# Kernel tuning notes

Hardware: AMD Instinct MI355X
Metric: run time of the kernel (lower is better)

## Reference

```python
import jax, jax.numpy as jnp
import numpy as np

WS = 4        # window_size
SHIFT = 3     # shift_size
HEADS = 4
DIM = 128
HR, WR = 256, 256  # input_resolution (matches post-upsample H, W)


def _rel_pos_index(ws):
    coords = np.stack(np.meshgrid(np.arange(ws), np.arange(ws), indexing='ij'))  # (2, ws, ws)
    cf = coords.reshape(2, -1)
    rel = (cf[:, :, None] - cf[:, None, :]).transpose(1, 2, 0).astype(np.int64)
    rel[:, :, 0] += ws - 1
    rel[:, :, 1] += ws - 1
    rel[:, :, 0] *= 2 * ws - 1
    return rel.sum(-1)  # (N, N)


def _attn_mask(H, W, ws, shift):
    img = np.zeros((H, W))
    cnt = 0
    sl = (slice(0, -ws), slice(-ws, -shift), slice(-shift, None))
    for hs in sl:
        for wsl in sl:
            img[hs, wsl] = cnt
            cnt += 1
    mw = img.reshape(H // ws, ws, W // ws, ws).transpose(0, 2, 1, 3).reshape(-1, ws * ws)
    diff = mw[:, None, :] - mw[:, :, None]  # unsqueeze(1) - unsqueeze(2)
    return np.where(diff != 0, -100.0, 0.0).astype(np.float32)  # (nW, N, N)


REL_IDX = jnp.asarray(_rel_pos_index(WS))
ATTN_MASK = jnp.asarray(_attn_mask(HR, WR, WS, SHIFT))


def _upsample2x_ac(x):
    def interp(x, axis):
        n = x.shape[axis]
        m = 2 * n
        pos = jnp.arange(m) * ((n - 1) / (m - 1))
        lo = jnp.floor(pos).astype(jnp.int32)
        hi = jnp.minimum(lo + 1, n - 1)
        w = (pos - lo).astype(x.dtype)
        shp = [1] * x.ndim
        shp[axis] = m
        w = w.reshape(shp)
        return jnp.take(x, lo, axis=axis) * (1 - w) + jnp.take(x, hi, axis=axis) * w
    return interp(interp(x, 2), 3)


def _conv2d(x, w, b, pad):
    y = jax.lax.conv_general_dilated(x, w, (1, 1), [(pad, pad), (pad, pad)],
                                     dimension_numbers=('NCHW', 'OIHW', 'NCHW'))
    return y + b[None, :, None, None]


def _bn(x, g, b, m, v):
    # eval-mode BatchNorm2d
    s = g / jnp.sqrt(v + 1e-5)
    return x * s[None, :, None, None] + (b - m * s)[None, :, None, None]


def setup_inputs():
    key = jax.random.key(0)
    ks = jax.random.split(key, 8)
    f = jax.random.normal
    return {
        'x': f(ks[0], (4, 256, 128, 64), jnp.float32),
        'qkv_w': f(ks[1], (DIM, 3 * DIM), jnp.float32) * 0.02,
        'qkv_b': jnp.zeros((3 * DIM,), jnp.float32),
        'proj_w': f(ks[2], (DIM, DIM), jnp.float32) * 0.02,
        'proj_b': jnp.zeros((DIM,), jnp.float32),
        'rpb': f(ks[3], ((2 * WS - 1) ** 2, HEADS), jnp.float32) * 0.02,
        'conv1_w': f(ks[4], (256, 256, 3, 3), jnp.float32) * 0.02,
        'conv1_b': jnp.zeros((256,), jnp.float32),
        'bn1_g': jnp.ones((256,), jnp.float32),
        'bn1_b': jnp.zeros((256,), jnp.float32),
        'bn1_m': jnp.zeros((256,), jnp.float32),
        'bn1_v': jnp.ones((256,), jnp.float32),
        'conv2_w': f(ks[5], (256, 256, 3, 3), jnp.float32) * 0.02,
        'conv2_b': jnp.zeros((256,), jnp.float32),
        'bn2_g': jnp.ones((256,), jnp.float32),
        'bn2_b': jnp.zeros((256,), jnp.float32),
        'bn2_m': jnp.zeros((256,), jnp.float32),
        'bn2_v': jnp.ones((256,), jnp.float32),
        'idc_w': f(ks[6], (256, 256, 1, 1), jnp.float32) * 0.02,
        'idc_b': jnp.zeros((256,), jnp.float32),
        'bni_g': jnp.ones((256,), jnp.float32),
        'bni_b': jnp.zeros((256,), jnp.float32),
        'bni_m': jnp.zeros((256,), jnp.float32),
        'bni_v': jnp.ones((256,), jnp.float32),
    }


def reference(x, qkv_w, qkv_b, proj_w, proj_b, rpb,
              conv1_w, conv1_b, bn1_g, bn1_b, bn1_m, bn1_v,
              conv2_w, conv2_b, bn2_g, bn2_b, bn2_m, bn2_v,
              idc_w, idc_b, bni_g, bni_b, bni_m, bni_v):
    x = _upsample2x_ac(x)                 # (B, 256, 256, 128), treated as (B,H,W,C) downstream
    B, H, W, C = x.shape
    shortcut = x
    xs = jnp.roll(x, (-SHIFT, -SHIFT), axis=(1, 2))
    # window partition -> (B*nW, N, C)
    nWh, nWw = H // WS, W // WS
    xw = xs.reshape(B, nWh, WS, nWw, WS, C).transpose(0, 1, 3, 2, 4, 5).reshape(-1, WS * WS, C)
    B_, N, _ = xw.shape
    hd = C // HEADS
    qkv = (xw @ qkv_w + qkv_b).reshape(B_, N, 3, HEADS, hd).transpose(2, 0, 3, 1, 4)
    q, k, v = qkv[0], qkv[1], qkv[2]
    attn = jnp.einsum('bhnd,bhmd->bhnm', q * (hd ** -0.5), k)
    bias = rpb[REL_IDX.reshape(-1)].reshape(N, N, HEADS).transpose(2, 0, 1)  # (h, N, N)
    attn = attn + bias[None]
    nW = ATTN_MASK.shape[0]
    attn = attn.reshape(B_ // nW, nW, HEADS, N, N) + ATTN_MASK[None, :, None]
    attn = jax.nn.softmax(attn.reshape(B_, HEADS, N, N), axis=-1)
    out = jnp.einsum('bhnm,bhmd->bhnd', attn, v).transpose(0, 2, 1, 3).reshape(B_, N, C)
    out = out @ proj_w + proj_b
    # window reverse + roll back
    out = out.reshape(B, nWh, nWw, WS, WS, C).transpose(0, 1, 3, 2, 4, 5).reshape(B, H, W, C)
    out = jnp.roll(out, (SHIFT, SHIFT), axis=(1, 2))
    x = shortcut + out
    # DoubleConv with identity branch (tensor treated as NCHW, per original code)
    y = _conv2d(x, conv1_w, conv1_b, 1)
    y = jax.nn.relu(_bn(y, bn1_g, bn1_b, bn1_m, bn1_v))
    y = _conv2d(y, conv2_w, conv2_b, 1)
    y = _bn(y, bn2_g, bn2_b, bn2_m, bn2_v)
    idn = _bn(_conv2d(x, idc_w, idc_b, 0), bni_g, bni_b, bni_m, bni_v)
    return jax.nn.relu(y + idn)
```

## Files before the change

kernel.cpp:

```cpp
#include <hip/hip_runtime.h>
#include <hip/hip_bf16.h>
#include <math.h>
#include <cstddef>

#define BATCH 4
#define WDIM 256
#define CDIM 128
#define WS 4
#define SHIFT 3
#define HEADS 4
#define HD 32
#define NTOK 16

typedef __attribute__((ext_vector_type(8))) short short8;
typedef __attribute__((ext_vector_type(4))) int int4v;
typedef __attribute__((ext_vector_type(4))) float f32x4;

__device__ __forceinline__ int regionOf(int v) {
    return v < (WDIM - WS) ? 0 : (v < (WDIM - SHIFT) ? 1 : 2);
}

__device__ __forceinline__ short f2bf(float v) {
    __hip_bfloat16 h = __float2bfloat16(v);
    return __builtin_bit_cast(short, h);
}
__device__ __forceinline__ float bf2f(short s) {
    unsigned u = ((unsigned)(unsigned short)s) << 16;
    return __builtin_bit_cast(float, u);
}

__global__ __launch_bounds__(256) void repack_attnw(
    const float* __restrict__ qkv_w,
    const float* __restrict__ proj_w,
    __hip_bfloat16* __restrict__ qkvw_rep,
    __hip_bfloat16* __restrict__ projw_rep)
{
    int idx = blockIdx.x * 256 + threadIdx.x;
    if (idx < 49152) {
        int j = idx >> 7, c = idx & 127;
        qkvw_rep[idx] = __float2bfloat16(qkv_w[c * 384 + j]);
    } else {
        int k = idx - 49152;
        int j = k >> 7, c = k & 127;
        projw_rep[k] = __float2bfloat16(proj_w[c * 128 + j]);
    }
}

#define XROW_RS 2114

__global__ __launch_bounds__(256, 4) void attn_kernel(
    const float* __restrict__ xin,
    const __hip_bfloat16* __restrict__ qkvw_rep,
    const __hip_bfloat16* __restrict__ projw_rep,
    const float* __restrict__ qkv_b,
    const float* __restrict__ proj_b,
    const float* __restrict__ rpb,
    __hip_bfloat16* __restrict__ xatt)
{
    __shared__ __align__(16) char smem[40864];
    float* xrowF  = (float*)smem;
    short* qkvs   = (short*)smem;
    short* aoutS  = (short*)smem;
    short* Xb     = (short*)(smem + 16912);
    short* Ps     = (short*)(smem + 25616);
    short* Vt     = (short*)(smem + 29712);
    float* rpbs   = (float*)(smem + 37904);
    float* qkvbS  = (float*)(smem + 38688);
    float* projbS = (float*)(smem + 40224);
    float* tokw2  = (float*)(smem + 40736);

    const int tid = threadIdx.x;
    const int bid = blockIdx.x;
    const int l   = tid & 63;
    const int wv  = tid >> 6;
    const int lm  = l & 15;
    const int lq  = l >> 4;

    if (tid < 196) rpbs[tid] = rpb[tid];
    for (int i = tid; i < 384; i += 256) qkvbS[i] = qkv_b[i];
    if (tid < 128) projbS[tid] = proj_b[tid];

    #pragma unroll
    for (int k = 0; k < 4; k++) {
        int id = tid + k * 256;
        int n   = id >> 5;
        int row = (id >> 4) & 1;
        int ll  = id & 15;
        int w_  = n >> 4, nn = n & 15;
        int win = bid * 2 + w_;
        int b   = win >> 12;
        int wh  = (win >> 6) & 63;
        int ww  = win & 63;
        int r = nn >> 2, c = nn & 3;
        int gh = (wh * 4 + r + SHIFT) & 255;
        int gw = (ww * 4 + c + SHIFT) & 255;
        float pos2 = gw * (127.0f / 255.0f);
        int lo2 = (int)floorf(pos2);
        int hi2 = min(lo2 + 1, 127);
        if (row == 0 && ll == 0) tokw2[n] = pos2 - (float)lo2;
        int src = row == 0 ? lo2 : hi2;
        const float4* rp = (const float4*)(xin + (((size_t)b * 256 + gh) * 128 + src) * 64);
        float4 v = rp[ll];
        float* bp = xrowF + row * XROW_RS + n + (4 * ll) * 33;
        bp[0]      = v.x;
        bp[33]     = v.y;
        bp[66]     = v.z;
        bp[99]     = v.w;
    }
    __syncthreads();

    {
        int n = tid >> 3;
        int jj = tid & 7;
        float w2 = tokw2[n];
        const float* x0 = xrowF + n;
        const float* x1 = x0 + XROW_RS;
        #pragma unroll
        for (int p = 0; p < 8; p++) {
            unsigned pk = 0;
            #pragma unroll
            for (int q = 0; q < 2; q++) {
                int cc = jj * 16 + p * 2 + q;
                float pos3 = cc * (63.0f / 127.0f);
                int lo3 = (int)floorf(pos3);
                float w3 = pos3 - (float)lo3;
                int o = lo3 * 33;
                float v0 = x0[o] * (1.f - w3) + x0[o + 33] * w3;
                float v1 = x1[o] * (1.f - w3) + x1[o + 33] * w3;
                float out = v0 * (1.f - w2) + v1 * w2;
                pk |= ((unsigned)(unsigned short)f2bf(out)) << (16 * q);
            }
            *(unsigned*)&Xb[n * 136 + jj * 16 + p * 2] = pk;
        }
    }
    __syncthreads();

    {
        f32x4 qacc[6][2];
        #pragma unroll
        for (int a = 0; a < 6; a++)
            #pragma unroll
            for (int t = 0; t < 2; t++) qacc[a][t] = (f32x4)0.0f;

        for (int ks = 0; ks < 4; ks++) {
            short8 af[6];
            #pragma unroll
            for (int jj = 0; jj < 6; jj++) {
                const int4v* gp = (const int4v*)(qkvw_rep +
                    (size_t)(wv * 96 + jj * 16 + lm) * 128 + ks * 32 + lq * 8);
                af[jj] = __builtin_bit_cast(short8, *gp);
            }
            short8 bfr[2];
            #pragma unroll
            for (int tt = 0; tt < 2; tt++)
                bfr[tt] = *(const short8*)&Xb[(tt * 16 + lm) * 136 + ks * 32 + lq * 8];
            #pragma unroll
            for (int jj = 0; jj < 6; jj++)
                #pragma unroll
                for (int tt = 0; tt < 2; tt++)
                    qacc[jj][tt] = __builtin_amdgcn_mfma_f32_16x16x32_bf16(
                        af[jj], bfr[tt], qacc[jj][tt], 0, 0, 0);
        }
        #pragma unroll
        for (int jj = 0; jj < 6; jj++) {
            int jbase = wv * 96 + jj * 16 + lq * 4;
            #pragma unroll
            for (int tt = 0; tt < 2; tt++) {
                int tok = tt * 16 + lm;
                if (jbase < 128) {
                    float v0 = (qacc[jj][tt][0] + qkvbS[jbase+0]) * 0.17677669529663687f;
                    float v1 = (qacc[jj][tt][1] + qkvbS[jbase+1]) * 0.17677669529663687f;
                    float v2 = (qacc[jj][tt][2] + qkvbS[jbase+2]) * 0.17677669529663687f;
                    float v3 = (qacc[jj][tt][3] + qkvbS[jbase+3]) * 0.17677669529663687f;
                    unsigned p0 = (unsigned short)f2bf(v0) | ((unsigned)(unsigned short)f2bf(v1) << 16);
                    unsigned p1 = (unsigned short)f2bf(v2) | ((unsigned)(unsigned short)f2bf(v3) << 16);
                    *(unsigned*)&qkvs[tok * 264 + jbase]     = p0;
                    *(unsigned*)&qkvs[tok * 264 + jbase + 2] = p1;
                } else if (jbase < 256) {
                    float v0 = qacc[jj][tt][0] + qkvbS[jbase+0];
                    float v1 = qacc[jj][tt][1] + qkvbS[jbase+1];
                    float v2 = qacc[jj][tt][2] + qkvbS[jbase+2];
                    float v3 = qacc[jj][tt][3] + qkvbS[jbase+3];
                    unsigned p0 = (unsigned short)f2bf(v0) | ((unsigned)(unsigned short)f2bf(v1) << 16);
                    unsigned p1 = (unsigned short)f2bf(v2) | ((unsigned)(unsigned short)f2bf(v3) << 16);
                    *(unsigned*)&qkvs[tok * 264 + jbase]     = p0;
                    *(unsigned*)&qkvs[tok * 264 + jbase + 2] = p1;
                } else {
                    #pragma unroll
                    for (int r = 0; r < 4; r++) {
                        int d = jbase - 256 + r;
                        Vt[(tt * 128 + d) * 16 + lm] = f2bf(qacc[jj][tt][r] + qkvbS[jbase + r]);
                    }
                }
            }
        }
    }
    __syncthreads();

    {
        int w_ = wv >> 1;
        int hb = (wv & 1) * 2;
        int win = bid * 2 + w_;
        int wh = (win >> 6) & 63;
        int ww = win & 63;
        int nq = lm;
        int r1 = nq >> 2, c1 = nq & 3;
        int reg1 = regionOf(wh * 4 + r1) * 3 + regionOf(ww * 4 + c1);
        #pragma unroll
        for (int hh = 0; hh < 2; hh++) {
            int h = hb + hh;
            short8 qa = *(const short8*)&qkvs[(w_ * 16 + lm) * 264 + h * 32 + lq * 8];
            short8 kb = *(const short8*)&qkvs[(w_ * 16 + lm) * 264 + 128 + h * 32 + lq * 8];
            f32x4 s = __builtin_amdgcn_mfma_f32_16x16x32_bf16(kb, qa, (f32x4)0.0f, 0, 0, 0);
            float v[4];
            #pragma unroll
            for (int r = 0; r < 4; r++) {
                int m = lq * 4 + r;
                int r2 = m >> 2, c2 = m & 3;
                int ridx = (r1 - r2 + 3) * 7 + (c1 - c2 + 3);
                v[r] = s[r] + rpbs[ridx * 4 + h];
                int reg2 = regionOf(wh * 4 + r2) * 3 + regionOf(ww * 4 + c2);
                if (reg2 != reg1) v[r] -= 100.f;
            }
            float mx = fmaxf(fmaxf(v[0], v[1]), fmaxf(v[2], v[3]));
            mx = fmaxf(mx, __shfl_xor(mx, 16));
            mx = fmaxf(mx, __shfl_xor(mx, 32));
            float e0 = __expf(v[0] - mx);
            float e1 = __expf(v[1] - mx);
            float e2 = __expf(v[2] - mx);
            float e3 = __expf(v[3] - mx);
            float ss = (e0 + e1) + (e2 + e3);
            ss += __shfl_xor(ss, 16);
            ss += __shfl_xor(ss, 32);
            float rinv = 1.0f / ss;
            unsigned plo = (unsigned short)f2bf(e0 * rinv) |
                           ((unsigned)(unsigned short)f2bf(e1 * rinv) << 16);
            unsigned phi = (unsigned short)f2bf(e2 * rinv) |
                           ((unsigned)(unsigned short)f2bf(e3 * rinv) << 16);
            unsigned long long pk = (unsigned long long)plo |
                                    ((unsigned long long)phi << 32);
            *(unsigned long long*)&Ps[((w_ * 4 + h) * 16 + lm) * 16 + lq * 4] = pk;
        }
    }
    __syncthreads();

    {
        int w_ = wv >> 1;
        int hb = (wv & 1) * 2;
        #pragma unroll
        for (int hh = 0; hh < 2; hh++) {
            int h = hb + hh;
            #pragma unroll
            for (int dt = 0; dt < 2; dt++) {
                short8 pa = (short8)0;
                short8 vb = (short8)0;
                if (lq < 2) {
                    pa = *(const short8*)&Ps[((w_ * 4 + h) * 16 + lm) * 16 + lq * 8];
                    vb = *(const short8*)&Vt[(w_ * 128 + h * 32 + dt * 16 + lm) * 16 + lq * 8];
                }
                f32x4 o = __builtin_amdgcn_mfma_f32_16x16x32_bf16(pa, vb, (f32x4)0.0f, 0, 0, 0);
                #pragma unroll
                for (int r = 0; r < 4; r++) {
                    aoutS[(w_ * 16 + lq * 4 + r) * 136 + h * 32 + dt * 16 + lm] = f2bf(o[r]);
                }
            }
        }
    }
    __syncthreads();

    {
        f32x4 cacc[2][2];
        #pragma unroll
        for (int a = 0; a < 2; a++)
            #pragma unroll
            for (int t = 0; t < 2; t++) cacc[a][t] = (f32x4)0.0f;

        for (int ks = 0; ks < 4; ks++) {
            short8 af[2];
            #pragma unroll
            for (int jj = 0; jj < 2; jj++) {
                const int4v* gp = (const int4v*)(projw_rep +
                    (size_t)(wv * 32 + jj * 16 + lm) * 128 + ks * 32 + lq * 8);
                af[jj] = __builtin_bit_cast(short8, *gp);
            }
            short8 bfr[2];
            #pragma unroll
            for (int tt = 0; tt < 2; tt++)
                bfr[tt] = *(const short8*)&aoutS[(tt * 16 + lm) * 136 + ks * 32 + lq * 8];
            #pragma unroll
            for (int jj = 0; jj < 2; jj++)
                #pragma unroll
                for (int tt = 0; tt < 2; tt++)
                    cacc[jj][tt] = __builtin_amdgcn_mfma_f32_16x16x32_bf16(
                        af[jj], bfr[tt], cacc[jj][tt], 0, 0, 0);
        }
        __syncthreads();
        #pragma unroll
        for (int jj = 0; jj < 2; jj++) {
            int jbase = wv * 32 + jj * 16 + lq * 4;
            #pragma unroll
            for (int tt = 0; tt < 2; tt++) {
                int tok = tt * 16 + lm;
                float v0 = cacc[jj][tt][0] + projbS[jbase+0] + bf2f(Xb[tok * 136 + jbase+0]);
                float v1 = cacc[jj][tt][1] + projbS[jbase+1] + bf2f(Xb[tok * 136 + jbase+1]);
                float v2 = cacc[jj][tt][2] + projbS[jbase+2] + bf2f(Xb[tok * 136 + jbase+2]);
                float v3 = cacc[jj][tt][3] + projbS[jbase+3] + bf2f(Xb[tok * 136 + jbase+3]);
                unsigned p0 = (unsigned short)f2bf(v0) | ((unsigned)(unsigned short)f2bf(v1) << 16);
                unsigned p1 = (unsigned short)f2bf(v2) | ((unsigned)(unsigned short)f2bf(v3) << 16);
                *(unsigned*)&aoutS[tok * 136 + jbase]     = p0;
                *(unsigned*)&aoutS[tok * 136 + jbase + 2] = p1;
            }
        }
    }
    __syncthreads();

    {
        #pragma unroll
        for (int k = 0; k < 4; k++) {
            int idx = k * 256 + tid;
            int j  = idx & 127;
            int c  = (idx >> 7) & 3;
            int w_ = idx >> 9;
            int win = bid * 2 + w_;
            int b   = win >> 12;
            int wh  = (win >> 6) & 63;
            int ww  = win & 63;
            int gw  = (ww * 4 + c + SHIFT) & 255;
            int slot0 = (wh * 4 + SHIFT + 1) & 255;
            unsigned short s0 = (unsigned short)aoutS[(w_ * 16 + 0 + c) * 136 + j];
            unsigned short s1 = (unsigned short)aoutS[(w_ * 16 + 4 + c) * 136 + j];
            unsigned short s2 = (unsigned short)aoutS[(w_ * 16 + 8 + c) * 136 + j];
            unsigned short s3 = (unsigned short)aoutS[(w_ * 16 + 12 + c) * 136 + j];
            unsigned long long pk =
                (unsigned long long)s0 | ((unsigned long long)s1 << 16) |
                ((unsigned long long)s2 << 32) | ((unsigned long long)s3 << 48);
            size_t base = (((size_t)b * 256 + gw) * 128 + j) * 256 + slot0;
            *(unsigned long long*)(xatt + base) = pk;
        }
    }
}

__global__ __launch_bounds__(256) void repack3(
    const float* __restrict__ w, const float* __restrict__ bias,
    const float* __restrict__ g_, const float* __restrict__ b_,
    const float* __restrict__ m_, const float* __restrict__ v_,
    __hip_bfloat16* __restrict__ wrep, float* __restrict__ cconst, int roll)
{
    int idx = blockIdx.x * 256 + threadIdx.x;
    int co = idx / 2304;
    int rem = idx - co * 2304;
    int ci = rem / 9;
    int tap = rem - ci * 9;
    float s = g_[co] * rsqrtf(v_[co] + 1e-5f);
    int ci_s = (ci + roll) & 255;
    size_t o = ((((size_t)(co >> 7) * 8 + (ci_s >> 5)) * 9 + tap) * 128 + (co & 127)) * 32 + (ci_s & 31);
    wrep[o] = __float2bfloat16(w[idx] * s);
    if (rem == 0) cconst[co] = bias[co] * s + (b_[co] - m_[co] * s);
}

__global__ __launch_bounds__(256) void repack1(
    const float* __restrict__ w, const float* __restrict__ bias,
    const float* __restrict__ g_, const float* __restrict__ b_,
    const float* __restrict__ m_, const float* __restrict__ v_,
    __hip_bfloat16* __restrict__ wrep, float* __restrict__ cconst)
{
    int idx = blockIdx.x * 256 + threadIdx.x;
    int co = idx >> 8, ci = idx & 255;
    float s = g_[co] * rsqrtf(v_[co] + 1e-5f);
    int ci_s = (ci + 1) & 255;
    wrep[(((size_t)(co >> 7) * 8 + (ci_s >> 5)) * 128 + (co & 127)) * 32 + (ci_s & 31)] =
        __float2bfloat16(w[idx] * s);
    if (ci == 0) cconst[co] += bias[co] * s + (b_[co] - m_[co] * s);
}

template<int HAS_IDC, int OUT_BF16>
__global__ __launch_bounds__(256) void conv_mfma(
    const __hip_bfloat16* __restrict__ xin,
    const __hip_bfloat16* __restrict__ xidc,
    const __hip_bfloat16* __restrict__ wrep,
    const __hip_bfloat16* __restrict__ wrepi,
    const float* __restrict__ cconst,
    void* __restrict__ outp)
{
    constexpr int NROWS = HAS_IDC ? 4 : 3;
    constexpr int NPER  = NROWS * 2;
    constexpr int NTAPS = HAS_IDC ? 10 : 9;
    __shared__ __align__(16) short xs[NROWS * 130 * 40];

    const int tid = threadIdx.x;
    const int l  = tid & 63;
    const int wv = tid >> 6;
    const int wave_co = (wv & 1) * 64;
    const int wave_w  = (wv >> 1) * 64;
    const int nb = ((blockIdx.x & 7) << 8) | (blockIdx.x >> 3);
    const int g = nb & 1;
    const int h = (nb >> 1) & 255;
    const int n = nb >> 9;
    const int lq = l >> 4;
    const int lm = l & 15;

    if (tid < 192) {
        int row = tid >> 6;
        int side = (tid >> 5) & 1;
        int ci = tid & 31;
        xs[(row * 130 + (side ? 129 : 0)) * 40 + ci] = 0;
    }

    f32x4 acc[4][4];
    #pragma unroll
    for (int a = 0; a < 4; a++)
        #pragma unroll
        for (int b = 0; b < 4; b++) acc[a][b] = (f32x4)0.0f;

    int4v pre[NPER];
    #pragma unroll
    for (int t = 0; t < NPER; t++) {
        int idx = t * 256 + tid;
        int c8  = idx & 3;
        int w   = (idx >> 2) & 127;
        int row = idx >> 9;
        int4v v = {0, 0, 0, 0};
        if (row < 3) {
            int hh = h - 1 + row;
            if (0 <= hh && hh < 256)
                v = *(const int4v*)(xin + ((((size_t)n * 256 + hh) * 128 + w) << 8) + c8 * 8);
        } else {
            v = *(const int4v*)(xidc + ((((size_t)n * 256 + h) * 128 + w) << 8) + c8 * 8);
        }
        pre[t] = v;
    }

    #pragma unroll 1
    for (int cb = 0; cb < 8; cb++) {
        __syncthreads();
        #pragma unroll
        for (int t = 0; t < NPER; t++) {
            int idx = t * 256 + tid;
            int c8  = idx & 3;
            int w   = (idx >> 2) & 127;
            int row = idx >> 9;
            *(int4v*)&xs[(row * 130 + w + 1) * 40 + c8 * 8] = pre[t];
        }
        __syncthreads();

        short8 afrA[4], afrB[4];
        auto loadW = [&](int tap, short8* afr) {
            const __hip_bfloat16* ap = (!HAS_IDC || tap < 9)
                ? wrep + ((((size_t)(g * 8 + cb) * 9 + tap)) << 12)
                : wrepi + (((size_t)(g * 8 + cb)) << 12);
            #pragma unroll
            for (int cs = 0; cs < 4; cs++)
                afr[cs] = __builtin_bit_cast(short8,
                    *(const int4v*)(ap + (size_t)(wave_co + cs * 16 + lm) * 32 + lq * 8));
        };
        auto computeT = [&](int tap, short8* afr) {
            const short* bs;
            if (HAS_IDC && tap == 9) {
                bs = xs + (3 * 130 + wave_w + 1) * 40;
            } else {
                int kh = tap / 3, kw = tap - kh * 3;
                bs = xs + (kh * 130 + wave_w + kw) * 40;
            }
            #pragma unroll
            for (int ws = 0; ws < 4; ws++) {
                short8 bfr = __builtin_bit_cast(short8,
                    *(const int4v*)&bs[(ws * 16 + lm) * 40 + lq * 8]);
                #pragma unroll
                for (int cs = 0; cs < 4; cs++)
                    acc[cs][ws] = __builtin_amdgcn_mfma_f32_16x16x32_bf16(
                        afr[cs], bfr, acc[cs][ws], 0, 0, 0);
            }
        };
        auto prefetch = [&]() {
            if (cb < 7) {
                #pragma unroll
                for (int t = 0; t < NPER; t++) {
                    int idx = t * 256 + tid;
                    int c8  = idx & 3;
                    int w   = (idx >> 2) & 127;
                    int row = idx >> 9;
                    int4v v = {0, 0, 0, 0};
                    if (row < 3) {
                        int hh = h - 1 + row;
                        if (0 <= hh && hh < 256)
                            v = *(const int4v*)(xin + ((((size_t)n * 256 + hh) * 128 + w) << 8)
                                                + (cb + 1) * 32 + c8 * 8);
                    } else {
                        v = *(const int4v*)(xidc + ((((size_t)n * 256 + h) * 128 + w) << 8)
                                            + (cb + 1) * 32 + c8 * 8);
                    }
                    pre[t] = v;
                }
            }
        };

        loadW(0, afrA);
        loadW(1, afrB);
        computeT(0, afrA);
        #pragma unroll 1
        for (int tap = 1; tap + 3 < NTAPS; tap += 2) {
            loadW(tap + 1, afrA);
            computeT(tap, afrB);
            loadW(tap + 2, afrB);
            computeT(tap + 1, afrA);
        }
        if constexpr (HAS_IDC) {
            loadW(8, afrA);
            computeT(7, afrB);
            loadW(9, afrB);
            prefetch();
            computeT(8, afrA);
            computeT(9, afrB);
        } else {
            loadW(8, afrA);
            prefetch();
            computeT(7, afrB);
            computeT(8, afrA);
        }
    }

    #pragma unroll
    for (int cs = 0; cs < 4; cs++) {
        int co0 = g * 128 + wave_co + cs * 16 + lq * 4;
        float c0 = cconst[co0 + 0], c1 = cconst[co0 + 1];
        float c2 = cconst[co0 + 2], c3 = cconst[co0 + 3];
        #pragma unroll
        for (int ws = 0; ws < 4; ws++) {
            int w = wave_w + ws * 16 + lm;
            float v0 = fmaxf(acc[cs][ws][0] + c0, 0.f);
            float v1 = fmaxf(acc[cs][ws][1] + c1, 0.f);
            float v2 = fmaxf(acc[cs][ws][2] + c2, 0.f);
            float v3 = fmaxf(acc[cs][ws][3] + c3, 0.f);
            if (OUT_BF16) {
                unsigned long long pk =
                    (unsigned long long)(unsigned short)f2bf(v0) |
                    ((unsigned long long)(unsigned short)f2bf(v1) << 16) |
                    ((unsigned long long)(unsigned short)f2bf(v2) << 32) |
                    ((unsigned long long)(unsigned short)f2bf(v3) << 48);
                size_t base = ((((size_t)n * 256 + h) * 128 + w) << 8) + co0;
                *(unsigned long long*)((__hip_bfloat16*)outp + base) = pk;
            } else {
                float* op = (float*)outp;
                op[(((size_t)n * 256 + co0 + 0) * 256 + h) * 128 + w] = v0;
                op[(((size_t)n * 256 + co0 + 1) * 256 + h) * 128 + w] = v1;
                op[(((size_t)n * 256 + co0 + 2) * 256 + h) * 128 + w] = v2;
                op[(((size_t)n * 256 + co0 + 3) * 256 + h) * 128 + w] = v3;
            }
        }
    }
}

extern "C" void kernel_launch(void* const* d_in, const int* in_sizes, int n_in,
                              void* d_out, int out_size, void* d_ws, size_t ws_size,
                              hipStream_t stream) {
    const float* x       = (const float*)d_in[0];
    const float* qkv_w   = (const float*)d_in[1];
    const float* qkv_b   = (const float*)d_in[2];
    const float* proj_w  = (const float*)d_in[3];
    const float* proj_b  = (const float*)d_in[4];
    const float* rpb     = (const float*)d_in[5];
    const float* conv1_w = (const float*)d_in[6];
    const float* conv1_b = (const float*)d_in[7];
    const float* bn1_g   = (const float*)d_in[8];
    const float* bn1_b   = (const float*)d_in[9];
    const float* bn1_m   = (const float*)d_in[10];
    const float* bn1_v   = (const float*)d_in[11];
    const float* conv2_w = (const float*)d_in[12];
    const float* conv2_b = (const float*)d_in[13];
    const float* bn2_g   = (const float*)d_in[14];
    const float* bn2_b   = (const float*)d_in[15];
    const float* bn2_m   = (const float*)d_in[16];
    const float* bn2_v   = (const float*)d_in[17];
    const float* idc_w   = (const float*)d_in[18];
    const float* idc_b   = (const float*)d_in[19];
    const float* bni_g   = (const float*)d_in[20];
    const float* bni_b   = (const float*)d_in[21];
    const float* bni_m   = (const float*)d_in[22];
    const float* bni_v   = (const float*)d_in[23];

    const size_t TE = (size_t)BATCH * 256 * 256 * 128;
    char* ws = (char*)d_ws;
    __hip_bfloat16* xatt  = (__hip_bfloat16*)(ws);
    __hip_bfloat16* y1    = (__hip_bfloat16*)(ws + TE * 2);
    __hip_bfloat16* wrep1 = (__hip_bfloat16*)(ws + TE * 4);
    __hip_bfloat16* wrep2 = (__hip_bfloat16*)(ws + TE * 4 + 1179648);
    __hip_bfloat16* wrepi = (__hip_bfloat16*)(ws + TE * 4 + 2359296);
    float*          c1    = (float*)(ws + TE * 4 + 2490368);
    float*          c2    = (float*)(ws + TE * 4 + 2491392);
    __hip_bfloat16* qkvw_rep = (__hip_bfloat16*)(ws + TE * 4 + 2492416);
    __hip_bfloat16* projw_rep= (__hip_bfloat16*)(ws + TE * 4 + 2590720);

    repack3<<<2304, 256, 0, stream>>>(conv1_w, conv1_b, bn1_g, bn1_b, bn1_m, bn1_v, wrep1, c1, 1);
    repack3<<<2304, 256, 0, stream>>>(conv2_w, conv2_b, bn2_g, bn2_b, bn2_m, bn2_v, wrep2, c2, 0);
    repack1<<<256, 256, 0, stream>>>(idc_w, idc_b, bni_g, bni_b, bni_m, bni_v, wrepi, c2);
    repack_attnw<<<256, 256, 0, stream>>>(qkv_w, proj_w, qkvw_rep, projw_rep);

    attn_kernel<<<8192, 256, 0, stream>>>(x, qkvw_rep, projw_rep, qkv_b, proj_b, rpb, xatt);

    conv_mfma<0, 1><<<2048, 256, 0, stream>>>(xatt, nullptr, wrep1, nullptr, c1, (void*)y1);
    conv_mfma<1, 0><<<2048, 256, 0, stream>>>(y1, xatt, wrep2, wrepi, c2, d_out);
}
```

Measured before the change: 719.3 us.

## Compute two output rows per conv block to reuse weights and halo rows

Each conv block now produces two output rows instead of one. It loads 4 (or 6 with the identity branch) input rows into shared memory and reuses every weight fragment across both rows, which halves the grid and cuts redundant weight and halo loads. The register prefetch of the next channel block and the double-buffered weight-fragment pipeline are removed, so global loads are no longer overlapped with MFMA work. Doubling the accumulators raises register pressure and may lower occupancy.

New measurement: 831.4 us. 1.16x slower.

```diff
diff --git a/kernel.cpp b/kernel.cpp
--- a/kernel.cpp
+++ b/kernel.cpp
@@ -382,7 +382,7 @@
     const float* __restrict__ cconst,
     void* __restrict__ outp)
 {
-    constexpr int NROWS = HAS_IDC ? 4 : 3;
+    constexpr int NROWS = HAS_IDC ? 6 : 4;
     constexpr int NPER  = NROWS * 2;
     constexpr int NTAPS = HAS_IDC ? 10 : 9;
     __shared__ __align__(16) short xs[NROWS * 130 * 40];
@@ -392,130 +392,91 @@
     const int wv = tid >> 6;
     const int wave_co = (wv & 1) * 64;
     const int wave_w  = (wv >> 1) * 64;
-    const int nb = ((blockIdx.x & 7) << 8) | (blockIdx.x >> 3);
-    const int g = nb & 1;
-    const int h = (nb >> 1) & 255;
-    const int n = nb >> 9;
+    const int nb = ((blockIdx.x & 7) << 7) | (blockIdx.x >> 3);
+    const int g  = nb & 1;
+    const int hp = (nb >> 1) & 127;
+    const int n  = nb >> 8;
+    const int h0 = hp * 2;
     const int lq = l >> 4;
     const int lm = l & 15;
 
-    if (tid < 192) {
-        int row = tid >> 6;
+    {
+        int row  = tid >> 6;
         int side = (tid >> 5) & 1;
-        int ci = tid & 31;
+        int ci   = tid & 31;
         xs[(row * 130 + (side ? 129 : 0)) * 40 + ci] = 0;
     }
 
-    f32x4 acc[4][4];
+    f32x4 acc[2][4][4];
     #pragma unroll
-    for (int a = 0; a < 4; a++)
-        #pragma unroll
-        for (int b = 0; b < 4; b++) acc[a][b] = (f32x4)0.0f;
-
-    int4v pre[NPER];
-    #pragma unroll
-    for (int t = 0; t < NPER; t++) {
-        int idx = t * 256 + tid;
-        int c8  = idx & 3;
-        int w   = (idx >> 2) & 127;
-        int row = idx >> 9;
-        int4v v = {0, 0, 0, 0};
-        if (row < 3) {
-            int hh = h - 1 + row;
-            if (0 <= hh && hh < 256)
-                v = *(const int4v*)(xin + ((((size_t)n * 256 + hh) * 128 + w) << 8) + c8 * 8);
-        } else {
-            v = *(const int4v*)(xidc + ((((size_t)n * 256 + h) * 128 + w) << 8) + c8 * 8);
-        }
-        pre[t] = v;
-    }
+    for (int r = 0; r < 2; r++)
+        #pragma unroll
+        for (int a = 0; a < 4; a++)
+            #pragma unroll
+            for (int b = 0; b < 4; b++) acc[r][a][b] = (f32x4)0.0f;
 
     #pragma unroll 1
     for (int cb = 0; cb < 8; cb++) {
         __syncthreads();
+        int4v tmp[NPER];
         #pragma unroll
         for (int t = 0; t < NPER; t++) {
             int idx = t * 256 + tid;
             int c8  = idx & 3;
             int w   = (idx >> 2) & 127;
             int row = idx >> 9;
-            *(int4v*)&xs[(row * 130 + w + 1) * 40 + c8 * 8] = pre[t];
+            int4v v = {0, 0, 0, 0};
+            if (!HAS_IDC || row < 4) {
+                int hh = h0 - 1 + row;
+                if (0 <= hh && hh < 256)
+                    v = *(const int4v*)(xin + ((((size_t)n * 256 + hh) * 128 + w) << 8)
+                                        + cb * 32 + c8 * 8);
+            } else {
+                int hh = h0 + (row - 4);
+                v = *(const int4v*)(xidc + ((((size_t)n * 256 + hh) * 128 + w) << 8)
+                                    + cb * 32 + c8 * 8);
+            }
+            tmp[t] = v;
+        }
+        #pragma unroll
+        for (int t = 0; t < NPER; t++) {
+            int idx = t * 256 + tid;
+            int c8  = idx & 3;
+            int w   = (idx >> 2) & 127;
+            int row = idx >> 9;
+            *(int4v*)&xs[(row * 130 + w + 1) * 40 + c8 * 8] = tmp[t];
         }
         __syncthreads();
 
-        short8 afrA[4], afrB[4];
-        auto loadW = [&](int tap, short8* afr) {
+        #pragma unroll 1
+        for (int tap = 0; tap < NTAPS; tap++) {
             const __hip_bfloat16* ap = (!HAS_IDC || tap < 9)
-                ? wrep + ((((size_t)(g * 8 + cb) * 9 + tap)) << 12)
+                ? wrep + (((size_t)(g * 8 + cb) * 9 + tap) << 12)
                 : wrepi + (((size_t)(g * 8 + cb)) << 12);
+            short8 afr[4];
             #pragma unroll
             for (int cs = 0; cs < 4; cs++)
                 afr[cs] = __builtin_bit_cast(short8,
                     *(const int4v*)(ap + (size_t)(wave_co + cs * 16 + lm) * 32 + lq * 8));
-        };
-        auto computeT = [&](int tap, short8* afr) {
-            const short* bs;
-            if (HAS_IDC && tap == 9) {
-                bs = xs + (3 * 130 + wave_w + 1) * 40;
-            } else {
-                int kh = tap / 3, kw = tap - kh * 3;
-                bs = xs + (kh * 130 + wave_w + kw) * 40;
-            }
-            #pragma unroll
-            for (int ws = 0; ws < 4; ws++) {
-                short8 bfr = __builtin_bit_cast(short8,
-                    *(const int4v*)&bs[(ws * 16 + lm) * 40 + lq * 8]);
+            #pragma unroll
+            for (int r = 0; r < 2; r++) {
+                const short* bs;
+                if (HAS_IDC && tap == 9) {
+                    bs = xs + ((4 + r) * 130 + wave_w + 1) * 40;
+                } else {
+                    int kh = tap / 3, kw = tap - kh * 3;
+                    bs = xs + ((kh + r) * 130 + wave_w + kw) * 40;
+                }
                 #pragma unroll
-                for (int cs = 0; cs < 4; cs++)
-                    acc[cs][ws] = __builtin_amdgcn_mfma_f32_16x16x32_bf16(
-                        afr[cs], bfr, acc[cs][ws], 0, 0, 0);
-            }
-        };
-        auto prefetch = [&]() {
-            if (cb < 7) {
-                #pragma unroll
-                for (int t = 0; t < NPER; t++) {
-                    int idx = t * 256 + tid;
-                    int c8  = idx & 3;
-                    int w   = (idx >> 2) & 127;
-                    int row = idx >> 9;
-                    int4v v = {0, 0, 0, 0};
-                    if (row < 3) {
-                        int hh = h - 1 + row;
-                        if (0 <= hh && hh < 256)
-                            v = *(const int4v*)(xin + ((((size_t)n * 256 + hh) * 128 + w) << 8)
-                                                + (cb + 1) * 32 + c8 * 8);
-                    } else {
-                        v = *(const int4v*)(xidc + ((((size_t)n * 256 + h) * 128 + w) << 8)
-                                            + (cb + 1) * 32 + c8 * 8);
-                    }
-                    pre[t] = v;
+                for (int ws = 0; ws < 4; ws++) {
+                    short8 bfr = __builtin_bit_cast(short8,
+                        *(const int4v*)&bs[(ws * 16 + lm) * 40 + lq * 8]);
+                    #pragma unroll
+                    for (int cs = 0; cs < 4; cs++)
+                        acc[r][cs][ws] = __builtin_amdgcn_mfma_f32_16x16x32_bf16(
+                            afr[cs], bfr, acc[r][cs][ws], 0, 0, 0);
                 }
             }
-        };
-
-        loadW(0, afrA);
-        loadW(1, afrB);
-        computeT(0, afrA);
-        #pragma unroll 1
-        for (int tap = 1; tap + 3 < NTAPS; tap += 2) {
-            loadW(tap + 1, afrA);
-            computeT(tap, afrB);
-            loadW(tap + 2, afrB);
-            computeT(tap + 1, afrA);
-        }
-        if constexpr (HAS_IDC) {
-            loadW(8, afrA);
-            computeT(7, afrB);
-            loadW(9, afrB);
-            prefetch();
-            computeT(8, afrA);
-            computeT(9, afrB);
-        } else {
-            loadW(8, afrA);
-            prefetch();
-            computeT(7, afrB);
-            computeT(8, afrA);
         }
     }
 
@@ -525,26 +486,30 @@
         float c0 = cconst[co0 + 0], c1 = cconst[co0 + 1];
         float c2 = cconst[co0 + 2], c3 = cconst[co0 + 3];
         #pragma unroll
-        for (int ws = 0; ws < 4; ws++) {
-            int w = wave_w + ws * 16 + lm;
-            float v0 = fmaxf(acc[cs][ws][0] + c0, 0.f);
-            float v1 = fmaxf(acc[cs][ws][1] + c1, 0.f);
-            float v2 = fmaxf(acc[cs][ws][2] + c2, 0.f);
-            float v3 = fmaxf(acc[cs][ws][3] + c3, 0.f);
-            if (OUT_BF16) {
-                unsigned long long pk =
-                    (unsigned long long)(unsigned short)f2bf(v0) |
-                    ((unsigned long long)(unsigned short)f2bf(v1) << 16) |
-                    ((unsigned long long)(unsigned short)f2bf(v2) << 32) |
-                    ((unsigned long long)(unsigned short)f2bf(v3) << 48);
-                size_t base = ((((size_t)n * 256 + h) * 128 + w) << 8) + co0;
-                *(unsigned long long*)((__hip_bfloat16*)outp + base) = pk;
-            } else {
-                float* op = (float*)outp;
-                op[(((size_t)n * 256 + co0 + 0) * 256 + h) * 128 + w] = v0;
-                op[(((size_t)n * 256 + co0 + 1) * 256 + h) * 128 + w] = v1;
-                op[(((size_t)n * 256 + co0 + 2) * 256 + h) * 128 + w] = v2;
-                op[(((size_t)n * 256 + co0 + 3) * 256 + h) * 128 + w] = v3;
+        for (int r = 0; r < 2; r++) {
+            int h = h0 + r;
+            #pragma unroll
+            for (int ws = 0; ws < 4; ws++) {
+                int w = wave_w + ws * 16 + lm;
+                float v0 = fmaxf(acc[r][cs][ws][0] + c0, 0.f);
+                float v1 = fmaxf(acc[r][cs][ws][1] + c1, 0.f);
+                float v2 = fmaxf(acc[r][cs][ws][2] + c2, 0.f);
+                float v3 = fmaxf(acc[r][cs][ws][3] + c3, 0.f);
+                if (OUT_BF16) {
+                    unsigned long long pk =
+                        (unsigned long long)(unsigned short)f2bf(v0) |
+                        ((unsigned long long)(unsigned short)f2bf(v1) << 16) |
+                        ((unsigned long long)(unsigned short)f2bf(v2) << 32) |
+                        ((unsigned long long)(unsigned short)f2bf(v3) << 48);
+                    size_t base = ((((size_t)n * 256 + h) * 128 + w) << 8) + co0;
+                    *(unsigned long long*)((__hip_bfloat16*)outp + base) = pk;
+                } else {
+                    float* op = (float*)outp;
+                    op[(((size_t)n * 256 + co0 + 0) * 256 + h) * 128 + w] = v0;
+                    op[(((size_t)n * 256 + co0 + 1) * 256 + h) * 128 + w] = v1;
+                    op[(((size_t)n * 256 + co0 + 2) * 256 + h) * 128 + w] = v2;
+                    op[(((size_t)n * 256 + co0 + 3) * 256 + h) * 128 + w] = v3;
+                }
             }
         }
     }
@@ -597,6 +562,6 @@
 
     attn_kernel<<<8192, 256, 0, stream>>>(x, qkvw_rep, projw_rep, qkv_b, proj_b, rpb, xatt);
 
-    conv_mfma<0, 1><<<2048, 256, 0, stream>>>(xatt, nullptr, wrep1, nullptr, c1, (void*)y1);
-    conv_mfma<1, 0><<<2048, 256, 0, stream>>>(y1, xatt, wrep2, wrepi, c2, d_out);
-}
+    conv_mfma<0, 1><<<1024, 256, 0, stream>>>(xatt, nullptr, wrep1, nullptr, c1, (void*)y1);
+    conv_mfma<1, 0><<<1024, 256, 0, stream>>>(y1, xatt, wrep2, wrepi, c2, d_out);
+}
```

## Split conv waves along width only and drop software-pipelined weight loads

Applied to the files above, without the earlier changes.

Each of the four waves now covers all 128 output channels over 32 width positions instead of a 64x64 channel-by-width quadrant. Each wave reads the full weight tile per tap and fewer activation fragments from shared memory. The double-buffered weight prefetch across taps is replaced by a plain per-tap load-then-compute loop, and the next channel block's global prefetch moves to the start of the iteration. This roughly doubles per-wave weight global/L2 traffic, and the simpler loop may expose load latency to the MFMAs.

Measured after the change: 954.7 us. +32.7%, slower.

```diff
diff --git a/kernel.cpp b/kernel.cpp
--- a/kernel.cpp
+++ b/kernel.cpp
@@ -390,8 +390,7 @@
     const int tid = threadIdx.x;
     const int l  = tid & 63;
     const int wv = tid >> 6;
-    const int wave_co = (wv & 1) * 64;
-    const int wave_w  = (wv >> 1) * 64;
+    const int wave_w = wv * 32;
     const int nb = ((blockIdx.x & 7) << 8) | (blockIdx.x >> 3);
     const int g = nb & 1;
     const int h = (nb >> 1) & 255;
@@ -406,11 +405,11 @@
         xs[(row * 130 + (side ? 129 : 0)) * 40 + ci] = 0;
     }
 
-    f32x4 acc[4][4];
+    f32x4 acc[8][2];
     #pragma unroll
-    for (int a = 0; a < 4; a++)
-        #pragma unroll
-        for (int b = 0; b < 4; b++) acc[a][b] = (f32x4)0.0f;
+    for (int a = 0; a < 8; a++)
+        #pragma unroll
+        for (int b = 0; b < 2; b++) acc[a][b] = (f32x4)0.0f;
 
     int4v pre[NPER];
     #pragma unroll
@@ -442,90 +441,66 @@
             *(int4v*)&xs[(row * 130 + w + 1) * 40 + c8 * 8] = pre[t];
         }
         __syncthreads();
-
-        short8 afrA[4], afrB[4];
-        auto loadW = [&](int tap, short8* afr) {
-            const __hip_bfloat16* ap = (!HAS_IDC || tap < 9)
-                ? wrep + ((((size_t)(g * 8 + cb) * 9 + tap)) << 12)
-                : wrepi + (((size_t)(g * 8 + cb)) << 12);
-            #pragma unroll
-            for (int cs = 0; cs < 4; cs++)
-                afr[cs] = __builtin_bit_cast(short8,
-                    *(const int4v*)(ap + (size_t)(wave_co + cs * 16 + lm) * 32 + lq * 8));
-        };
-        auto computeT = [&](int tap, short8* afr) {
+        if (cb < 7) {
+            #pragma unroll
+            for (int t = 0; t < NPER; t++) {
+                int idx = t * 256 + tid;
+                int c8  = idx & 3;
+                int w   = (idx >> 2) & 127;
+                int row = idx >> 9;
+                int4v v = {0, 0, 0, 0};
+                if (row < 3) {
+                    int hh = h - 1 + row;
+                    if (0 <= hh && hh < 256)
+                        v = *(const int4v*)(xin + ((((size_t)n * 256 + hh) * 128 + w) << 8)
+                                            + (cb + 1) * 32 + c8 * 8);
+                } else {
+                    v = *(const int4v*)(xidc + ((((size_t)n * 256 + h) * 128 + w) << 8)
+                                        + (cb + 1) * 32 + c8 * 8);
+                }
+                pre[t] = v;
+            }
+        }
+
+        #pragma unroll 1
+        for (int tap = 0; tap < NTAPS; tap++) {
+            const __hip_bfloat16* ap;
             const short* bs;
-            if (HAS_IDC && tap == 9) {
+            if (!HAS_IDC || tap < 9) {
+                int kh = tap / 3;
+                int kw = tap - kh * 3;
+                ap = wrep + ((((size_t)(g * 8 + cb) * 9 + tap)) << 12);
+                bs = xs + (kh * 130 + wave_w + kw) * 40;
+            } else {
+                ap = wrepi + (((size_t)(g * 8 + cb)) << 12);
                 bs = xs + (3 * 130 + wave_w + 1) * 40;
-            } else {
-                int kh = tap / 3, kw = tap - kh * 3;
-                bs = xs + (kh * 130 + wave_w + kw) * 40;
-            }
-            #pragma unroll
-            for (int ws = 0; ws < 4; ws++) {
+            }
+            short8 afr[8];
+            #pragma unroll
+            for (int cs = 0; cs < 8; cs++) {
+                const int4v* p4 = (const int4v*)(ap + (size_t)(cs * 16 + lm) * 32 + lq * 8);
+                afr[cs] = __builtin_bit_cast(short8, *p4);
+            }
+            #pragma unroll
+            for (int ws = 0; ws < 2; ws++) {
                 short8 bfr = __builtin_bit_cast(short8,
                     *(const int4v*)&bs[(ws * 16 + lm) * 40 + lq * 8]);
                 #pragma unroll
-                for (int cs = 0; cs < 4; cs++)
+                for (int cs = 0; cs < 8; cs++) {
                     acc[cs][ws] = __builtin_amdgcn_mfma_f32_16x16x32_bf16(
                         afr[cs], bfr, acc[cs][ws], 0, 0, 0);
-            }
-        };
-        auto prefetch = [&]() {
-            if (cb < 7) {
-                #pragma unroll
-                for (int t = 0; t < NPER; t++) {
-                    int idx = t * 256 + tid;
-                    int c8  = idx & 3;
-                    int w   = (idx >> 2) & 127;
-                    int row = idx >> 9;
-                    int4v v = {0, 0, 0, 0};
-                    if (row < 3) {
-                        int hh = h - 1 + row;
-                        if (0 <= hh && hh < 256)
-                            v = *(const int4v*)(xin + ((((size_t)n * 256 + hh) * 128 + w) << 8)
-                                                + (cb + 1) * 32 + c8 * 8);
-                    } else {
-                        v = *(const int4v*)(xidc + ((((size_t)n * 256 + h) * 128 + w) << 8)
-                                            + (cb + 1) * 32 + c8 * 8);
-                    }
-                    pre[t] = v;
                 }
             }
-        };
-
-        loadW(0, afrA);
-        loadW(1, afrB);
-        computeT(0, afrA);
-        #pragma unroll 1
-        for (int tap = 1; tap + 3 < NTAPS; tap += 2) {
-            loadW(tap + 1, afrA);
-            computeT(tap, afrB);
-            loadW(tap + 2, afrB);
-            computeT(tap + 1, afrA);
-        }
-        if constexpr (HAS_IDC) {
-            loadW(8, afrA);
-            computeT(7, afrB);
-            loadW(9, afrB);
-            prefetch();
-            computeT(8, afrA);
-            computeT(9, afrB);
-        } else {
-            loadW(8, afrA);
-            prefetch();
-            computeT(7, afrB);
-            computeT(8, afrA);
         }
     }
 
     #pragma unroll
-    for (int cs = 0; cs < 4; cs++) {
-        int co0 = g * 128 + wave_co + cs * 16 + lq * 4;
+    for (int cs = 0; cs < 8; cs++) {
+        int co0 = g * 128 + cs * 16 + lq * 4;
         float c0 = cconst[co0 + 0], c1 = cconst[co0 + 1];
         float c2 = cconst[co0 + 2], c3 = cconst[co0 + 3];
         #pragma unroll
-        for (int ws = 0; ws < 4; ws++) {
+        for (int ws = 0; ws < 2; ws++) {
             int w = wave_w + ws * 16 + lm;
             float v0 = fmaxf(acc[cs][ws][0] + c0, 0.f);
             float v1 = fmaxf(acc[cs][ws][1] + c1, 0.f);
```
